# Kernel optimization log

Measured on AMD Instinct MI355X. Metric: run time of the kernel, lower is better.

## Reference

```python
import jax, jax.numpy as jnp
import numpy as np

D_MODEL = 1024
N_HEADS = 16
D_HEAD = D_MODEL // N_HEADS
EPS = 1e-6


def setup_inputs() -> dict:
    key = jax.random.key(0)
    ks = jax.random.split(key, 11)
    N, L, S = 4, 4096, 4096
    scale = 1.0 / np.sqrt(D_MODEL)
    inp = {
        "queries": jax.random.normal(ks[0], (N, L, D_MODEL), jnp.float32),
        "keys": jax.random.normal(ks[1], (N, S, D_MODEL), jnp.float32),
        "values": jax.random.normal(ks[2], (N, S, D_MODEL), jnp.float32),
        "Wq": jax.random.normal(ks[3], (D_MODEL, D_MODEL), jnp.float32) * scale,
        "bq": jnp.zeros((D_MODEL,), jnp.float32),
        "Wk": jax.random.normal(ks[4], (D_MODEL, D_MODEL), jnp.float32) * scale,
        "bk": jnp.zeros((D_MODEL,), jnp.float32),
        "Wv": jax.random.normal(ks[5], (D_MODEL, D_MODEL), jnp.float32) * scale,
        "bv": jnp.zeros((D_MODEL,), jnp.float32),
        "Wo": jax.random.normal(ks[6], (D_MODEL, D_MODEL), jnp.float32) * scale,
        "bo": jnp.zeros((D_MODEL,), jnp.float32),
    }
    return inp


def reference(queries, keys, values, Wq, bq, Wk, bk, Wv, bv, Wo, bo):
    N, L, _ = queries.shape
    S = keys.shape[1]
    H, Dh = N_HEADS, D_HEAD
    # projections (torch Linear: x @ W.T + b)
    q = (queries @ Wq.T + bq).reshape(N, L, H, Dh)
    k = (keys @ Wk.T + bk).reshape(N, S, H, Dh)
    v = (values @ Wv.T + bv).reshape(N, S, H, Dh)
    # elu+1 feature map
    Q = jax.nn.elu(q) + 1.0
    K = jax.nn.elu(k) + 1.0
    # KV summary: [N,H,Dv,Dh]
    KV = jnp.einsum('nshd,nshm->nhmd', K, v)
    # normalizer: [N,L,H]
    Z = 1.0 / (jnp.einsum('nlhd,nhd->nlh', Q, K.sum(axis=1)) + EPS)
    # output per head: [N,L,H,Dv]
    V = jnp.einsum('nlhd,nhmd,nlh->nlhm', Q, KV, Z)
    out = V.reshape(N, L, H * Dh) @ Wo.T + bo
    return out
```

## Files before the change

kernel.cpp:

```cpp
#include <hip/hip_runtime.h>
#include <hip/hip_bf16.h>

typedef __attribute__((ext_vector_type(8))) short short8;
typedef __attribute__((ext_vector_type(4))) short short4v;
typedef __attribute__((ext_vector_type(4))) float f32x4;

#define MFMA16(a, b, c) __builtin_amdgcn_mfma_f32_16x16x32_bf16(a, b, c, 0, 0, 0)

__device__ __forceinline__ unsigned short f2bf(float f) {
    unsigned int u = __float_as_uint(f);
    unsigned int r = u + 0x7fffu + ((u >> 16) & 1u);
    return (unsigned short)(r >> 16);
}
__device__ __forceinline__ float bf2f(unsigned short h) {
    return __uint_as_float(((unsigned int)h) << 16);
}

__device__ __forceinline__ void async16(const void* g, void* l) {
    __builtin_amdgcn_global_load_lds(
        (const __attribute__((address_space(1))) unsigned int*)g,
        (__attribute__((address_space(3))) unsigned int*)l, 16, 0, 0);
}

#define S_BARRIER() asm volatile("s_barrier" ::: "memory")
#define SCHED_FENCE() __builtin_amdgcn_sched_barrier(0)

__global__ __launch_bounds__(256) void cvt_kernel(const float* __restrict__ in,
                                                  unsigned short* __restrict__ out,
                                                  int n4) {
    int i = blockIdx.x * 256 + threadIdx.x;
    int stride = gridDim.x * 256;
    for (; i < n4; i += stride) {
        float4 v = reinterpret_cast<const float4*>(in)[i];
        short4v p;
        p[0] = (short)f2bf(v.x); p[1] = (short)f2bf(v.y);
        p[2] = (short)f2bf(v.z); p[3] = (short)f2bf(v.w);
        reinterpret_cast<short4v*>(out)[i] = p;
    }
}

template <int MODE>
__global__ __launch_bounds__(512, 2) void gemm8p(const unsigned short* __restrict__ A,
                                                 const unsigned short* __restrict__ B,
                                                 const float* __restrict__ bias,
                                                 void* __restrict__ out) {
    __shared__ __align__(16) char lds[131072];

    const int tid = threadIdx.x;
    const int lane = tid & 63, wid = tid >> 6;
    const int wr = wid >> 2, wc = wid & 3;
    const int lr = lane & 15, lg = lane >> 4;

    const int nwg = gridDim.x;
    const int bid = blockIdx.x;
    const int swz = (bid & 7) * (nwg >> 3) + (bid >> 3);
    const int bm = swz >> 2, bn = swz & 3;
    const long row0 = (long)bm * 256;
    const long col0 = (long)bn * 256;

    const unsigned short* srcA[2];
    const unsigned short* srcB[2];
    int dstOff[2];
#pragma unroll
    for (int g = 0; g < 2; ++g) {
        int s = g * 512 + tid;
        int pr = s >> 3;
        int dc = (s & 7) ^ (pr & 7);
        srcA[g] = A + (row0 + (pr & 63) + 128 * (pr >> 6)) * 1024 + dc * 8;
        srcB[g] = B + (col0 + pr) * 1024 + dc * 8;
        dstOff[g] = s * 16;
    }

#define STG_AQ(BB, Q, KT) do {                                                  \
        async16(srcA[0] + (Q) * 65536 + (KT) * 64,                              \
                lds + (BB) * 65536 + (Q) * 16384 + dstOff[0]);                  \
        async16(srcA[1] + (Q) * 65536 + (KT) * 64,                              \
                lds + (BB) * 65536 + (Q) * 16384 + dstOff[1]); } while (0)
#define STG_BH(BB, H, KT) do {                                                  \
        async16(srcB[0] + (H) * 131072 + (KT) * 64,                             \
                lds + (BB) * 65536 + 32768 + (H) * 16384 + dstOff[0]);          \
        async16(srcB[1] + (H) * 131072 + (KT) * 64,                             \
                lds + (BB) * 65536 + 32768 + (H) * 16384 + dstOff[1]); } while (0)

    const int ch0 = (((0 * 4 + lg) ^ (lr & 7)) << 4);
    const int ch1 = (((1 * 4 + lg) ^ (lr & 7)) << 4);
    const int aB0 = (64 * wr + lr) * 128 + ch0;
    const int aB1 = (64 * wr + lr) * 128 + ch1;
    const int bB0 = 32768 + (wc >> 1) * 16384 + ((wc & 1) * 64 + lr) * 128 + ch0;
    const int bB1 = 32768 + (wc >> 1) * 16384 + ((wc & 1) * 64 + lr) * 128 + ch1;

    f32x4 acc[8][4] = {};
    short8 b0[4], b1[4];

#define GATE4() do { asm volatile("s_waitcnt vmcnt(4)" ::: "memory"); SCHED_FENCE(); } while (0)
#define GATE0() do { asm volatile("s_waitcnt vmcnt(0)" ::: "memory"); SCHED_FENCE(); } while (0)
#define MFMA_BLOCK(MB, BV) do {                                                 \
        S_BARRIER();                                                            \
        asm volatile("s_waitcnt lgkmcnt(0)" ::: "memory");                      \
        SCHED_FENCE();                                                          \
        __builtin_amdgcn_s_setprio(1);                                          \
        _Pragma("unroll") for (int m = 0; m < 4; ++m)                           \
            _Pragma("unroll") for (int n = 0; n < 4; ++n)                       \
                acc[(MB) + m][n] = MFMA16(a[m], BV[n], acc[(MB) + m][n]);       \
        __builtin_amdgcn_s_setprio(0);                                          \
        SCHED_FENCE();                                                          \
        S_BARRIER(); } while (0)
#define LOAD_A(BUFB, ABASE, Q) do {                                             \
        _Pragma("unroll") for (int m = 0; m < 4; ++m)                           \
            a[m] = *(const short8*)(lds + (BUFB) + (Q) * 16384 + (ABASE) + m * 2048); } while (0)
#define LOAD_B(BUFB, BBASE, BV) do {                                            \
        _Pragma("unroll") for (int n = 0; n < 4; ++n)                           \
            BV[n] = *(const short8*)(lds + (BUFB) + (BBASE) + n * 2048); } while (0)

    STG_AQ(0, 0, 0); STG_BH(0, 0, 0); STG_BH(0, 1, 0); STG_AQ(0, 1, 0);
    STG_AQ(1, 0, 1); STG_BH(1, 0, 1);
    GATE4();
    S_BARRIER();

#pragma unroll 1
    for (int t = 0; t < 7; ++t) {
        const int ktA = 2 * t + 1, ktB = 2 * t + 2, ktC = 2 * t + 3;
        {
            short8 a[4];
            LOAD_B(0, bB0, b0); LOAD_A(0, aB0, 0);
            STG_BH(1, 1, ktA);
            MFMA_BLOCK(0, b0);
        }
        {
            short8 a[4];
            LOAD_B(0, bB1, b1); LOAD_A(0, aB1, 0);
            STG_AQ(1, 1, ktA);
            MFMA_BLOCK(0, b1);
        }
        {
            short8 a[4];
            LOAD_A(0, aB0, 1);
            STG_AQ(0, 0, ktB);
            MFMA_BLOCK(4, b0);
        }
        {
            short8 a[4];
            LOAD_A(0, aB1, 1);
            STG_BH(0, 0, ktB);
            GATE4();
            MFMA_BLOCK(4, b1);
        }
        {
            short8 a[4];
            LOAD_B(65536, bB0, b0); LOAD_A(65536, aB0, 0);
            STG_BH(0, 1, ktB);
            MFMA_BLOCK(0, b0);
        }
        {
            short8 a[4];
            LOAD_B(65536, bB1, b1); LOAD_A(65536, aB1, 0);
            STG_AQ(0, 1, ktB);
            MFMA_BLOCK(0, b1);
        }
        {
            short8 a[4];
            LOAD_A(65536, aB0, 1);
            STG_AQ(1, 0, ktC);
            MFMA_BLOCK(4, b0);
        }
        {
            short8 a[4];
            LOAD_A(65536, aB1, 1);
            STG_BH(1, 0, ktC);
            GATE4();
            MFMA_BLOCK(4, b1);
        }
    }
    {
        { short8 a[4]; LOAD_B(0, bB0, b0); LOAD_A(0, aB0, 0); STG_BH(1, 1, 15); MFMA_BLOCK(0, b0); }
        { short8 a[4]; LOAD_B(0, bB1, b1); LOAD_A(0, aB1, 0); STG_AQ(1, 1, 15); MFMA_BLOCK(0, b1); }
        { short8 a[4]; LOAD_A(0, aB0, 1); MFMA_BLOCK(4, b0); }
        { short8 a[4]; LOAD_A(0, aB1, 1); GATE0(); MFMA_BLOCK(4, b1); }
        { short8 a[4]; LOAD_B(65536, bB0, b0); LOAD_A(65536, aB0, 0); MFMA_BLOCK(0, b0); }
        { short8 a[4]; LOAD_B(65536, bB1, b1); LOAD_A(65536, aB1, 0); MFMA_BLOCK(0, b1); }
        { short8 a[4]; LOAD_A(65536, aB0, 1); MFMA_BLOCK(4, b0); }
        { short8 a[4]; LOAD_A(65536, aB1, 1); MFMA_BLOCK(4, b1); }
    }
#undef STG_AQ
#undef STG_BH
#undef GATE4
#undef GATE0
#undef MFMA_BLOCK
#undef LOAD_A
#undef LOAD_B

    const int r4 = lg * 4;
#pragma unroll
    for (int m = 0; m < 8; ++m) {
#pragma unroll
        for (int n = 0; n < 4; ++n) {
            long col = col0 + wc * 64 + n * 16 + lr;
            float bcol = bias[col];
            long R0 = row0 + wr * 128 + m * 16 + r4;
            if (MODE == 0) {
                unsigned short* O = (unsigned short*)out;
#pragma unroll
                for (int j = 0; j < 4; ++j) {
                    float v = acc[m][n][j] + bcol;
                    v = v > 0.f ? v + 1.f : __expf(v);
                    O[(R0 + j) * 1024 + col] = f2bf(v);
                }
            } else if (MODE == 1 || MODE == 2) {
                unsigned short* O = (unsigned short*)out;
                long nb = R0 >> 12;
                long s = R0 & 4095;
                short4v pack;
#pragma unroll
                for (int j = 0; j < 4; ++j) {
                    float v = acc[m][n][j] + bcol;
                    if (MODE == 1) v = v > 0.f ? v + 1.f : __expf(v);
                    pack[j] = (short)f2bf(v);
                }
                *(short4v*)(O + ((nb << 10) + col) * 4096 + s) = pack;
            } else {
                float* O = (float*)out;
#pragma unroll
                for (int j = 0; j < 4; ++j)
                    O[(R0 + j) * 1024 + col] = acc[m][n][j] + bcol;
            }
        }
    }
}

__global__ __launch_bounds__(256) void kv_kernel(const unsigned short* __restrict__ Kt,
                                                 const unsigned short* __restrict__ vT,
                                                 float* __restrict__ KV,
                                                 float* __restrict__ Ksum) {
    int b = blockIdx.x;
    int sc = b & 7, h = (b >> 3) & 15, n = b >> 7;
    const int tid = threadIdx.x, lane = tid & 63, wave = tid >> 6;
    long base = ((long)(n * 1024 + h * 64)) * 4096 + sc * 512;
    const unsigned short* Kp = Kt + base;
    const unsigned short* Vp = vT + base;
    const int lr = lane & 15, lk = (lane >> 4) * 8;

    f32x4 acc[4] = {};
    for (int s0 = 0; s0 < 512; s0 += 32) {
        short8 a = *(const short8*)(Vp + (long)(wave * 16 + lr) * 4096 + s0 + lk);
#pragma unroll
        for (int d4 = 0; d4 < 4; ++d4) {
            short8 bb = *(const short8*)(Kp + (long)(d4 * 16 + lr) * 4096 + s0 + lk);
            acc[d4] = MFMA16(a, bb, acc[d4]);
        }
    }
    float* KVb = KV + (long)(n * 16 + h) * 4096;
#pragma unroll
    for (int d4 = 0; d4 < 4; ++d4)
#pragma unroll
        for (int j = 0; j < 4; ++j) {
            int m = wave * 16 + (lane >> 4) * 4 + j;
            int d = d4 * 16 + lr;
            atomicAdd(KVb + m * 64 + d, acc[d4][j]);
        }
    int d = tid & 63, part = tid >> 6;
    const unsigned short* kp2 = Kt + ((long)(n * 1024 + h * 64 + d)) * 4096 + sc * 512 + part * 128;
    float s = 0.f;
    for (int i = 0; i < 128; i += 8) {
        short8 v = *(const short8*)(kp2 + i);
#pragma unroll
        for (int e = 0; e < 8; ++e) s += bf2f((unsigned short)v[e]);
    }
    atomicAdd(Ksum + n * 1024 + h * 64 + d, s);
}

__global__ __launch_bounds__(256) void attn_kernel(const unsigned short* __restrict__ Qm,
                                                   const float* __restrict__ KV,
                                                   const float* __restrict__ Ksum,
                                                   unsigned short* __restrict__ Vbuf) {
    __shared__ unsigned short Qs[128 * 64];
    __shared__ unsigned short KVs[64 * 64];
    __shared__ float zin[128];
    __shared__ float ks[64];
    int b = blockIdx.x;
    int lc = b & 31, h = (b >> 5) & 15, n = b >> 9;
    int tid = threadIdx.x, lane = tid & 63, wave = tid >> 6;
    long l0 = (long)n * 4096 + lc * 128;

    const unsigned short* Qg = Qm + (l0 + (tid >> 3)) * 1024 + h * 64 + (tid & 7) * 8;
    char* QsB = (char*)Qs + (wave << 10);
#pragma unroll
    for (int it = 0; it < 4; ++it)
        async16(Qg + (long)it * 32 * 1024, QsB + it * 4096);

    const float* kvp = KV + (long)(n * 16 + h) * 4096;
    for (int i = tid * 4; i < 4096; i += 1024) {
        float4 v = *reinterpret_cast<const float4*>(kvp + i);
        short4v p;
        p[0] = (short)f2bf(v.x); p[1] = (short)f2bf(v.y);
        p[2] = (short)f2bf(v.z); p[3] = (short)f2bf(v.w);
        *(short4v*)(KVs + i) = p;
    }
    if (tid < 64) ks[tid] = Ksum[n * 1024 + h * 64 + tid];
    __syncthreads();

    if (tid < 128) {
        float den = 0.f;
        const unsigned short* qrow = Qs + tid * 64;
#pragma unroll
        for (int d = 0; d < 64; ++d) den += bf2f(qrow[d]) * ks[d];
        zin[tid] = 1.0f / (den + 1e-6f);
    }
    __syncthreads();

    const int lr = lane & 15, lk = (lane >> 4) * 8;
    f32x4 acc[2][4] = {};
#pragma unroll
    for (int kk = 0; kk < 2; ++kk) {
        short8 a0 = *(const short8*)(Qs + (wave * 32 + lr) * 64 + kk * 32 + lk);
        short8 a1 = *(const short8*)(Qs + (wave * 32 + 16 + lr) * 64 + kk * 32 + lk);
#pragma unroll
        for (int nn = 0; nn < 4; ++nn) {
            short8 bb = *(const short8*)(KVs + (nn * 16 + lr) * 64 + kk * 32 + lk);
            acc[0][nn] = MFMA16(a0, bb, acc[0][nn]);
            acc[1][nn] = MFMA16(a1, bb, acc[1][nn]);
        }
    }
#pragma unroll
    for (int mi = 0; mi < 2; ++mi)
#pragma unroll
        for (int nn = 0; nn < 4; ++nn)
#pragma unroll
            for (int j = 0; j < 4; ++j) {
                int rl = wave * 32 + mi * 16 + (lane >> 4) * 4 + j;
                int mcol = nn * 16 + lr;
                float v = acc[mi][nn][j] * zin[rl];
                Vbuf[(l0 + rl) * 1024 + h * 64 + mcol] = f2bf(v);
            }
}

extern "C" void kernel_launch(void* const* d_in, const int* in_sizes, int n_in,
                              void* d_out, int out_size, void* d_ws, size_t ws_size,
                              hipStream_t stream) {
    const float* queries = (const float*)d_in[0];
    const float* keys    = (const float*)d_in[1];
    const float* values  = (const float*)d_in[2];
    const float* Wq = (const float*)d_in[3];
    const float* bq = (const float*)d_in[4];
    const float* Wk = (const float*)d_in[5];
    const float* bk = (const float*)d_in[6];
    const float* Wv = (const float*)d_in[7];
    const float* bv = (const float*)d_in[8];
    const float* Wo = (const float*)d_in[9];
    const float* bo = (const float*)d_in[10];
    float* out = (float*)d_out;

    char* ws = (char*)d_ws;
    const size_t SZ = (size_t)16384 * 1024 * 2;
    const size_t WSZ = (size_t)1024 * 1024 * 2;
    unsigned short* qb  = (unsigned short*)(ws);
    unsigned short* kb  = (unsigned short*)(ws + SZ);
    unsigned short* vb  = (unsigned short*)(ws + 2 * SZ);
    unsigned short* Wqb = (unsigned short*)(ws + 3 * SZ);
    unsigned short* Wkb = (unsigned short*)(ws + 3 * SZ + WSZ);
    unsigned short* Wvb = (unsigned short*)(ws + 3 * SZ + 2 * WSZ);
    unsigned short* Wob = (unsigned short*)(ws + 3 * SZ + 3 * WSZ);
    unsigned short* Qm  = (unsigned short*)(ws + 3 * SZ + 4 * WSZ);
    unsigned short* Kt  = (unsigned short*)(ws + 4 * SZ + 4 * WSZ);
    unsigned short* vT  = (unsigned short*)(ws + 5 * SZ + 4 * WSZ);
    float* KVf = (float*)(ws + 6 * SZ + 4 * WSZ);
    float* Ksf = (float*)(ws + 6 * SZ + 4 * WSZ + 1048576);
    unsigned short* Vbuf = qb;

    const int n4big = 16384 * 1024 / 4;
    const int n4w = 1024 * 1024 / 4;
    cvt_kernel<<<2048, 256, 0, stream>>>(queries, qb, n4big);
    cvt_kernel<<<2048, 256, 0, stream>>>(keys, kb, n4big);
    cvt_kernel<<<2048, 256, 0, stream>>>(values, vb, n4big);
    cvt_kernel<<<256, 256, 0, stream>>>(Wq, Wqb, n4w);
    cvt_kernel<<<256, 256, 0, stream>>>(Wk, Wkb, n4w);
    cvt_kernel<<<256, 256, 0, stream>>>(Wv, Wvb, n4w);
    cvt_kernel<<<256, 256, 0, stream>>>(Wo, Wob, n4w);

    gemm8p<0><<<256, 512, 0, stream>>>(qb, Wqb, bq, Qm);
    gemm8p<1><<<256, 512, 0, stream>>>(kb, Wkb, bk, Kt);
    gemm8p<2><<<256, 512, 0, stream>>>(vb, Wvb, bv, vT);

    hipMemsetAsync(KVf, 0, 1048576 + 16384, stream);
    kv_kernel<<<512, 256, 0, stream>>>(Kt, vT, KVf, Ksf);
    attn_kernel<<<2048, 256, 0, stream>>>(Qm, KVf, Ksf, Vbuf);

    gemm8p<3><<<256, 512, 0, stream>>>(Vbuf, Wob, bo, out);
}
```

Baseline: 273.0 us.

## Fuse fp32-to-bf16 activation conversion into projection GEMM A-tile loads

The Q/K/V projection GEMMs now read fp32 activations directly: each thread loads float4 pairs into registers, packs them to bf16 and writes them to LDS, which replaces the async global-to-LDS copies for the A operand. This drops three separate conversion kernels that each read 64MB of fp32 and wrote 32MB of bf16, along with the GEMM's later re-read of that bf16. The four weight conversions are also merged into one launch. The cost is register pressure from the prefetch buffers, extra VALU packing work inside the pipelined main loop, and double-width global reads for A.

```diff
diff --git a/kernel.cpp b/kernel.cpp
--- a/kernel.cpp
+++ b/kernel.cpp
@@ -15,6 +15,9 @@
 __device__ __forceinline__ float bf2f(unsigned short h) {
     return __uint_as_float(((unsigned int)h) << 16);
 }
+__device__ __forceinline__ unsigned int pk2(float lo, float hi) {
+    return (unsigned int)f2bf(lo) | ((unsigned int)f2bf(hi) << 16);
+}
 
 __device__ __forceinline__ void async16(const void* g, void* l) {
     __builtin_amdgcn_global_load_lds(
@@ -25,12 +28,20 @@
 #define S_BARRIER() asm volatile("s_barrier" ::: "memory")
 #define SCHED_FENCE() __builtin_amdgcn_sched_barrier(0)
 
-__global__ __launch_bounds__(256) void cvt_kernel(const float* __restrict__ in,
-                                                  unsigned short* __restrict__ out,
-                                                  int n4) {
-    int i = blockIdx.x * 256 + threadIdx.x;
-    int stride = gridDim.x * 256;
-    for (; i < n4; i += stride) {
+__global__ __launch_bounds__(256) void cvt4_kernel(const float* __restrict__ w0,
+                                                   const float* __restrict__ w1,
+                                                   const float* __restrict__ w2,
+                                                   const float* __restrict__ w3,
+                                                   unsigned short* __restrict__ o0,
+                                                   unsigned short* __restrict__ o1,
+                                                   unsigned short* __restrict__ o2,
+                                                   unsigned short* __restrict__ o3,
+                                                   int n4) {
+    int wsel = blockIdx.x >> 7;
+    int lb = blockIdx.x & 127;
+    const float* in = wsel == 0 ? w0 : wsel == 1 ? w1 : wsel == 2 ? w2 : w3;
+    unsigned short* out = wsel == 0 ? o0 : wsel == 1 ? o1 : wsel == 2 ? o2 : o3;
+    for (int i = lb * 256 + threadIdx.x; i < n4; i += 32768) {
         float4 v = reinterpret_cast<const float4*>(in)[i];
         short4v p;
         p[0] = (short)f2bf(v.x); p[1] = (short)f2bf(v.y);
@@ -39,8 +50,8 @@
     }
 }
 
-template <int MODE>
-__global__ __launch_bounds__(512, 2) void gemm8p(const unsigned short* __restrict__ A,
+template <int MODE, int AFP32>
+__global__ __launch_bounds__(512, 2) void gemm8p(const void* __restrict__ Araw,
                                                  const unsigned short* __restrict__ B,
                                                  const float* __restrict__ bias,
                                                  void* __restrict__ out) {
@@ -58,7 +69,8 @@
     const long row0 = (long)bm * 256;
     const long col0 = (long)bn * 256;
 
-    const unsigned short* srcA[2];
+    const int ESZ = AFP32 ? 4 : 2;
+    const char* srcAbase[2];
     const unsigned short* srcB[2];
     int dstOff[2];
 #pragma unroll
@@ -66,21 +78,35 @@
         int s = g * 512 + tid;
         int pr = s >> 3;
         int dc = (s & 7) ^ (pr & 7);
-        srcA[g] = A + (row0 + (pr & 63) + 128 * (pr >> 6)) * 1024 + dc * 8;
+        srcAbase[g] = (const char*)Araw +
+                      (long)((row0 + (pr & 63) + 128 * (pr >> 6)) * 1024 + dc * 8) * ESZ;
         srcB[g] = B + (col0 + pr) * 1024 + dc * 8;
         dstOff[g] = s * 16;
     }
 
 #define STG_AQ(BB, Q, KT) do {                                                  \
-        async16(srcA[0] + (Q) * 65536 + (KT) * 64,                              \
+        async16(srcAbase[0] + ((Q) * 65536 + (KT) * 64) * 2,                    \
                 lds + (BB) * 65536 + (Q) * 16384 + dstOff[0]);                  \
-        async16(srcA[1] + (Q) * 65536 + (KT) * 64,                              \
+        async16(srcAbase[1] + ((Q) * 65536 + (KT) * 64) * 2,                    \
                 lds + (BB) * 65536 + (Q) * 16384 + dstOff[1]); } while (0)
 #define STG_BH(BB, H, KT) do {                                                  \
         async16(srcB[0] + (H) * 131072 + (KT) * 64,                             \
                 lds + (BB) * 65536 + 32768 + (H) * 16384 + dstOff[0]);          \
         async16(srcB[1] + (H) * 131072 + (KT) * 64,                             \
                 lds + (BB) * 65536 + 32768 + (H) * 16384 + dstOff[1]); } while (0)
+#define A_ISSUE(ARR, Q, KT) do {                                                \
+        const char* s0_ = srcAbase[0] + ((Q) * 65536 + (KT) * 64) * 4;          \
+        const char* s1_ = srcAbase[1] + ((Q) * 65536 + (KT) * 64) * 4;          \
+        ARR[0] = *(const float4*)s0_;  ARR[1] = *(const float4*)(s0_ + 16);     \
+        ARR[2] = *(const float4*)s1_;  ARR[3] = *(const float4*)(s1_ + 16); } while (0)
+#define A_PACK(ARR, BB, Q) do {                                                 \
+        uint4 w0_, w1_;                                                         \
+        w0_.x = pk2(ARR[0].x, ARR[0].y); w0_.y = pk2(ARR[0].z, ARR[0].w);       \
+        w0_.z = pk2(ARR[1].x, ARR[1].y); w0_.w = pk2(ARR[1].z, ARR[1].w);       \
+        w1_.x = pk2(ARR[2].x, ARR[2].y); w1_.y = pk2(ARR[2].z, ARR[2].w);       \
+        w1_.z = pk2(ARR[3].x, ARR[3].y); w1_.w = pk2(ARR[3].z, ARR[3].w);       \
+        *(uint4*)(lds + (BB) * 65536 + (Q) * 16384 + dstOff[0]) = w0_;          \
+        *(uint4*)(lds + (BB) * 65536 + (Q) * 16384 + dstOff[1]) = w1_; } while (0)
 
     const int ch0 = (((0 * 4 + lg) ^ (lr & 7)) << 4);
     const int ch1 = (((1 * 4 + lg) ^ (lr & 7)) << 4);
@@ -91,8 +117,11 @@
 
     f32x4 acc[8][4] = {};
     short8 b0[4], b1[4];
-
-#define GATE4() do { asm volatile("s_waitcnt vmcnt(4)" ::: "memory"); SCHED_FENCE(); } while (0)
+    float4 apreA[4], apreB[4];
+
+#define GATEN() do { if (AFP32) asm volatile("s_waitcnt vmcnt(6)" ::: "memory");     \
+                     else       asm volatile("s_waitcnt vmcnt(4)" ::: "memory");     \
+                     SCHED_FENCE(); } while (0)
 #define GATE0() do { asm volatile("s_waitcnt vmcnt(0)" ::: "memory"); SCHED_FENCE(); } while (0)
 #define MFMA_BLOCK(MB, BV) do {                                                 \
         S_BARRIER();                                                            \
@@ -112,10 +141,24 @@
         _Pragma("unroll") for (int n = 0; n < 4; ++n)                           \
             BV[n] = *(const short8*)(lds + (BUFB) + (BBASE) + n * 2048); } while (0)
 
-    STG_AQ(0, 0, 0); STG_BH(0, 0, 0); STG_BH(0, 1, 0); STG_AQ(0, 1, 0);
-    STG_AQ(1, 0, 1); STG_BH(1, 0, 1);
-    GATE4();
-    S_BARRIER();
+    if (AFP32) {
+        STG_BH(0, 0, 0); STG_BH(0, 1, 0); STG_BH(1, 0, 1);
+        float4 t0[4], t1[4], t2[4];
+        A_ISSUE(t0, 0, 0); A_ISSUE(t1, 1, 0);
+        A_PACK(t0, 0, 0);
+        A_ISSUE(t2, 0, 1);
+        A_PACK(t1, 0, 1);
+        A_PACK(t2, 1, 0);
+        A_ISSUE(apreA, 1, 1);
+        asm volatile("s_waitcnt lgkmcnt(0)" ::: "memory");
+        SCHED_FENCE();
+        S_BARRIER();
+    } else {
+        STG_AQ(0, 0, 0); STG_BH(0, 0, 0); STG_BH(0, 1, 0); STG_AQ(0, 1, 0);
+        STG_AQ(1, 0, 1); STG_BH(1, 0, 1);
+        GATEN();
+        S_BARRIER();
+    }
 
 #pragma unroll 1
     for (int t = 0; t < 7; ++t) {
@@ -129,20 +172,22 @@
         {
             short8 a[4];
             LOAD_B(0, bB1, b1); LOAD_A(0, aB1, 0);
-            STG_AQ(1, 1, ktA);
+            if (AFP32) { A_ISSUE(apreB, 0, ktB); A_PACK(apreA, 1, 1); }
+            else       { STG_AQ(1, 1, ktA); }
             MFMA_BLOCK(0, b1);
         }
         {
             short8 a[4];
             LOAD_A(0, aB0, 1);
-            STG_AQ(0, 0, ktB);
+            if (AFP32) { A_ISSUE(apreA, 1, ktB); A_PACK(apreB, 0, 0); }
+            else       { STG_AQ(0, 0, ktB); }
             MFMA_BLOCK(4, b0);
         }
         {
             short8 a[4];
             LOAD_A(0, aB1, 1);
             STG_BH(0, 0, ktB);
-            GATE4();
+            GATEN();
             MFMA_BLOCK(4, b1);
         }
         {
@@ -154,26 +199,30 @@
         {
             short8 a[4];
             LOAD_B(65536, bB1, b1); LOAD_A(65536, aB1, 0);
-            STG_AQ(0, 1, ktB);
+            if (AFP32) { A_ISSUE(apreB, 0, ktC); A_PACK(apreA, 0, 1); }
+            else       { STG_AQ(0, 1, ktB); }
             MFMA_BLOCK(0, b1);
         }
         {
             short8 a[4];
             LOAD_A(65536, aB0, 1);
-            STG_AQ(1, 0, ktC);
+            if (AFP32) { A_ISSUE(apreA, 1, ktC); A_PACK(apreB, 1, 0); }
+            else       { STG_AQ(1, 0, ktC); }
             MFMA_BLOCK(4, b0);
         }
         {
             short8 a[4];
             LOAD_A(65536, aB1, 1);
             STG_BH(1, 0, ktC);
-            GATE4();
+            GATEN();
             MFMA_BLOCK(4, b1);
         }
     }
     {
         { short8 a[4]; LOAD_B(0, bB0, b0); LOAD_A(0, aB0, 0); STG_BH(1, 1, 15); MFMA_BLOCK(0, b0); }
-        { short8 a[4]; LOAD_B(0, bB1, b1); LOAD_A(0, aB1, 0); STG_AQ(1, 1, 15); MFMA_BLOCK(0, b1); }
+        { short8 a[4]; LOAD_B(0, bB1, b1); LOAD_A(0, aB1, 0);
+          if (AFP32) { A_PACK(apreA, 1, 1); } else { STG_AQ(1, 1, 15); }
+          MFMA_BLOCK(0, b1); }
         { short8 a[4]; LOAD_A(0, aB0, 1); MFMA_BLOCK(4, b0); }
         { short8 a[4]; LOAD_A(0, aB1, 1); GATE0(); MFMA_BLOCK(4, b1); }
         { short8 a[4]; LOAD_B(65536, bB0, b0); LOAD_A(65536, aB0, 0); MFMA_BLOCK(0, b0); }
@@ -183,7 +232,9 @@
     }
 #undef STG_AQ
 #undef STG_BH
-#undef GATE4
+#undef A_ISSUE
+#undef A_PACK
+#undef GATEN
 #undef GATE0
 #undef MFMA_BLOCK
 #undef LOAD_A
@@ -352,37 +403,27 @@
     char* ws = (char*)d_ws;
     const size_t SZ = (size_t)16384 * 1024 * 2;
     const size_t WSZ = (size_t)1024 * 1024 * 2;
-    unsigned short* qb  = (unsigned short*)(ws);
-    unsigned short* kb  = (unsigned short*)(ws + SZ);
-    unsigned short* vb  = (unsigned short*)(ws + 2 * SZ);
-    unsigned short* Wqb = (unsigned short*)(ws + 3 * SZ);
-    unsigned short* Wkb = (unsigned short*)(ws + 3 * SZ + WSZ);
-    unsigned short* Wvb = (unsigned short*)(ws + 3 * SZ + 2 * WSZ);
-    unsigned short* Wob = (unsigned short*)(ws + 3 * SZ + 3 * WSZ);
-    unsigned short* Qm  = (unsigned short*)(ws + 3 * SZ + 4 * WSZ);
-    unsigned short* Kt  = (unsigned short*)(ws + 4 * SZ + 4 * WSZ);
-    unsigned short* vT  = (unsigned short*)(ws + 5 * SZ + 4 * WSZ);
-    float* KVf = (float*)(ws + 6 * SZ + 4 * WSZ);
-    float* Ksf = (float*)(ws + 6 * SZ + 4 * WSZ + 1048576);
-    unsigned short* Vbuf = qb;
-
-    const int n4big = 16384 * 1024 / 4;
+    unsigned short* Wqb = (unsigned short*)(ws);
+    unsigned short* Wkb = (unsigned short*)(ws + WSZ);
+    unsigned short* Wvb = (unsigned short*)(ws + 2 * WSZ);
+    unsigned short* Wob = (unsigned short*)(ws + 3 * WSZ);
+    unsigned short* Qm   = (unsigned short*)(ws + 4 * WSZ);
+    unsigned short* Kt   = (unsigned short*)(ws + 4 * WSZ + SZ);
+    unsigned short* vT   = (unsigned short*)(ws + 4 * WSZ + 2 * SZ);
+    unsigned short* Vbuf = (unsigned short*)(ws + 4 * WSZ + 3 * SZ);
+    float* KVf = (float*)(ws + 4 * WSZ + 4 * SZ);
+    float* Ksf = (float*)(ws + 4 * WSZ + 4 * SZ + 1048576);
+
     const int n4w = 1024 * 1024 / 4;
-    cvt_kernel<<<2048, 256, 0, stream>>>(queries, qb, n4big);
-    cvt_kernel<<<2048, 256, 0, stream>>>(keys, kb, n4big);
-    cvt_kernel<<<2048, 256, 0, stream>>>(values, vb, n4big);
-    cvt_kernel<<<256, 256, 0, stream>>>(Wq, Wqb, n4w);
-    cvt_kernel<<<256, 256, 0, stream>>>(Wk, Wkb, n4w);
-    cvt_kernel<<<256, 256, 0, stream>>>(Wv, Wvb, n4w);
-    cvt_kernel<<<256, 256, 0, stream>>>(Wo, Wob, n4w);
-
-    gemm8p<0><<<256, 512, 0, stream>>>(qb, Wqb, bq, Qm);
-    gemm8p<1><<<256, 512, 0, stream>>>(kb, Wkb, bk, Kt);
-    gemm8p<2><<<256, 512, 0, stream>>>(vb, Wvb, bv, vT);
+    cvt4_kernel<<<512, 256, 0, stream>>>(Wq, Wk, Wv, Wo, Wqb, Wkb, Wvb, Wob, n4w);
+
+    gemm8p<0, 1><<<256, 512, 0, stream>>>(queries, Wqb, bq, Qm);
+    gemm8p<1, 1><<<256, 512, 0, stream>>>(keys, Wkb, bk, Kt);
+    gemm8p<2, 1><<<256, 512, 0, stream>>>(values, Wvb, bv, vT);
 
     hipMemsetAsync(KVf, 0, 1048576 + 16384, stream);
     kv_kernel<<<512, 256, 0, stream>>>(Kt, vT, KVf, Ksf);
     attn_kernel<<<2048, 256, 0, stream>>>(Qm, KVf, Ksf, Vbuf);
 
-    gemm8p<3><<<256, 512, 0, stream>>>(Vbuf, Wob, bo, out);
-}
+    gemm8p<3, 0><<<256, 512, 0, stream>>>(Vbuf, Wob, bo, out);
+}
```

Result: slower. 289.9 us (+6.2%).

## Merge conversion launches and batch Q/K/V projection GEMMs into single kernels

Applied to the files above, without the earlier changes.

Replaces seven separate fp32-to-bf16 conversion launches with one kernel that dispatches by block index, and merges the three projection GEMMs into one 768-block launch that picks its operands per segment. This is meant to remove launch gaps and tail underutilization between the small kernels. The GEMM body becomes a device function with a runtime mode, which may add branching in the epilogue. Launch bounds change from 2 to 1 blocks per SM. The attention kernel also spreads the normalizer dot product across all 256 threads with a shuffle reduction instead of 128 threads.

```diff
diff --git a/kernel.cpp b/kernel.cpp
--- a/kernel.cpp
+++ b/kernel.cpp
@@ -25,35 +25,56 @@
 #define S_BARRIER() asm volatile("s_barrier" ::: "memory")
 #define SCHED_FENCE() __builtin_amdgcn_sched_barrier(0)
 
-__global__ __launch_bounds__(256) void cvt_kernel(const float* __restrict__ in,
-                                                  unsigned short* __restrict__ out,
-                                                  int n4) {
-    int i = blockIdx.x * 256 + threadIdx.x;
-    int stride = gridDim.x * 256;
-    for (; i < n4; i += stride) {
-        float4 v = reinterpret_cast<const float4*>(in)[i];
+__global__ __launch_bounds__(256) void cvt_all(const float* __restrict__ q,
+                                               const float* __restrict__ k,
+                                               const float* __restrict__ v,
+                                               const float* __restrict__ Wq,
+                                               const float* __restrict__ Wk,
+                                               const float* __restrict__ Wv,
+                                               const float* __restrict__ Wo,
+                                               unsigned short* __restrict__ qb,
+                                               unsigned short* __restrict__ kb,
+                                               unsigned short* __restrict__ vb,
+                                               unsigned short* __restrict__ Wqb,
+                                               unsigned short* __restrict__ Wkb,
+                                               unsigned short* __restrict__ Wvb,
+                                               unsigned short* __restrict__ Wob) {
+    int b = blockIdx.x;
+    const float* in;
+    unsigned short* out;
+    int lb, nb, n4;
+    if (b < 6144) {
+        int s = b >> 11;
+        lb = b & 2047; nb = 2048; n4 = 4194304;
+        in = s == 0 ? q : s == 1 ? k : v;
+        out = s == 0 ? qb : s == 1 ? kb : vb;
+    } else {
+        int s = b - 6144;
+        int w = s >> 7;
+        lb = s & 127; nb = 128; n4 = 262144;
+        in = w == 0 ? Wq : w == 1 ? Wk : w == 2 ? Wv : Wo;
+        out = w == 0 ? Wqb : w == 1 ? Wkb : w == 2 ? Wvb : Wob;
+    }
+    for (int i = lb * 256 + threadIdx.x; i < n4; i += nb * 256) {
+        float4 vv = reinterpret_cast<const float4*>(in)[i];
         short4v p;
-        p[0] = (short)f2bf(v.x); p[1] = (short)f2bf(v.y);
-        p[2] = (short)f2bf(v.z); p[3] = (short)f2bf(v.w);
+        p[0] = (short)f2bf(vv.x); p[1] = (short)f2bf(vv.y);
+        p[2] = (short)f2bf(vv.z); p[3] = (short)f2bf(vv.w);
         reinterpret_cast<short4v*>(out)[i] = p;
     }
 }
 
-template <int MODE>
-__global__ __launch_bounds__(512, 2) void gemm8p(const unsigned short* __restrict__ A,
-                                                 const unsigned short* __restrict__ B,
-                                                 const float* __restrict__ bias,
-                                                 void* __restrict__ out) {
-    __shared__ __align__(16) char lds[131072];
-
+__device__ __forceinline__ void gemm_body(const unsigned short* __restrict__ A,
+                                          const unsigned short* __restrict__ B,
+                                          const float* __restrict__ bias,
+                                          void* __restrict__ out,
+                                          int mode, char* lds, int bid) {
     const int tid = threadIdx.x;
     const int lane = tid & 63, wid = tid >> 6;
     const int wr = wid >> 2, wc = wid & 3;
     const int lr = lane & 15, lg = lane >> 4;
 
-    const int nwg = gridDim.x;
-    const int bid = blockIdx.x;
-    const int swz = (bid & 7) * (nwg >> 3) + (bid >> 3);
+    const int swz = (bid & 7) * 32 + (bid >> 3);
     const int bm = swz >> 2, bn = swz & 3;
     const long row0 = (long)bm * 256;
     const long col0 = (long)bn * 256;
@@ -120,56 +141,14 @@
 #pragma unroll 1
     for (int t = 0; t < 7; ++t) {
         const int ktA = 2 * t + 1, ktB = 2 * t + 2, ktC = 2 * t + 3;
-        {
-            short8 a[4];
-            LOAD_B(0, bB0, b0); LOAD_A(0, aB0, 0);
-            STG_BH(1, 1, ktA);
-            MFMA_BLOCK(0, b0);
-        }
-        {
-            short8 a[4];
-            LOAD_B(0, bB1, b1); LOAD_A(0, aB1, 0);
-            STG_AQ(1, 1, ktA);
-            MFMA_BLOCK(0, b1);
-        }
-        {
-            short8 a[4];
-            LOAD_A(0, aB0, 1);
-            STG_AQ(0, 0, ktB);
-            MFMA_BLOCK(4, b0);
-        }
-        {
-            short8 a[4];
-            LOAD_A(0, aB1, 1);
-            STG_BH(0, 0, ktB);
-            GATE4();
-            MFMA_BLOCK(4, b1);
-        }
-        {
-            short8 a[4];
-            LOAD_B(65536, bB0, b0); LOAD_A(65536, aB0, 0);
-            STG_BH(0, 1, ktB);
-            MFMA_BLOCK(0, b0);
-        }
-        {
-            short8 a[4];
-            LOAD_B(65536, bB1, b1); LOAD_A(65536, aB1, 0);
-            STG_AQ(0, 1, ktB);
-            MFMA_BLOCK(0, b1);
-        }
-        {
-            short8 a[4];
-            LOAD_A(65536, aB0, 1);
-            STG_AQ(1, 0, ktC);
-            MFMA_BLOCK(4, b0);
-        }
-        {
-            short8 a[4];
-            LOAD_A(65536, aB1, 1);
-            STG_BH(1, 0, ktC);
-            GATE4();
-            MFMA_BLOCK(4, b1);
-        }
+        { short8 a[4]; LOAD_B(0, bB0, b0); LOAD_A(0, aB0, 0); STG_BH(1, 1, ktA); MFMA_BLOCK(0, b0); }
+        { short8 a[4]; LOAD_B(0, bB1, b1); LOAD_A(0, aB1, 0); STG_AQ(1, 1, ktA); MFMA_BLOCK(0, b1); }
+        { short8 a[4]; LOAD_A(0, aB0, 1); STG_AQ(0, 0, ktB); MFMA_BLOCK(4, b0); }
+        { short8 a[4]; LOAD_A(0, aB1, 1); STG_BH(0, 0, ktB); GATE4(); MFMA_BLOCK(4, b1); }
+        { short8 a[4]; LOAD_B(65536, bB0, b0); LOAD_A(65536, aB0, 0); STG_BH(0, 1, ktB); MFMA_BLOCK(0, b0); }
+        { short8 a[4]; LOAD_B(65536, bB1, b1); LOAD_A(65536, aB1, 0); STG_AQ(0, 1, ktB); MFMA_BLOCK(0, b1); }
+        { short8 a[4]; LOAD_A(65536, aB0, 1); STG_AQ(1, 0, ktC); MFMA_BLOCK(4, b0); }
+        { short8 a[4]; LOAD_A(65536, aB1, 1); STG_BH(1, 0, ktC); GATE4(); MFMA_BLOCK(4, b1); }
     }
     {
         { short8 a[4]; LOAD_B(0, bB0, b0); LOAD_A(0, aB0, 0); STG_BH(1, 1, 15); MFMA_BLOCK(0, b0); }
@@ -197,7 +176,7 @@
             long col = col0 + wc * 64 + n * 16 + lr;
             float bcol = bias[col];
             long R0 = row0 + wr * 128 + m * 16 + r4;
-            if (MODE == 0) {
+            if (mode == 0) {
                 unsigned short* O = (unsigned short*)out;
 #pragma unroll
                 for (int j = 0; j < 4; ++j) {
@@ -205,7 +184,7 @@
                     v = v > 0.f ? v + 1.f : __expf(v);
                     O[(R0 + j) * 1024 + col] = f2bf(v);
                 }
-            } else if (MODE == 1 || MODE == 2) {
+            } else if (mode == 1 || mode == 2) {
                 unsigned short* O = (unsigned short*)out;
                 long nb = R0 >> 12;
                 long s = R0 & 4095;
@@ -213,7 +192,7 @@
 #pragma unroll
                 for (int j = 0; j < 4; ++j) {
                     float v = acc[m][n][j] + bcol;
-                    if (MODE == 1) v = v > 0.f ? v + 1.f : __expf(v);
+                    if (mode == 1) v = v > 0.f ? v + 1.f : __expf(v);
                     pack[j] = (short)f2bf(v);
                 }
                 *(short4v*)(O + ((nb << 10) + col) * 4096 + s) = pack;
@@ -225,6 +204,36 @@
             }
         }
     }
+}
+
+__global__ __launch_bounds__(512, 1) void proj_gemm(const unsigned short* __restrict__ qb,
+                                                    const unsigned short* __restrict__ kb,
+                                                    const unsigned short* __restrict__ vb,
+                                                    const unsigned short* __restrict__ Wqb,
+                                                    const unsigned short* __restrict__ Wkb,
+                                                    const unsigned short* __restrict__ Wvb,
+                                                    const float* __restrict__ bq,
+                                                    const float* __restrict__ bk,
+                                                    const float* __restrict__ bv,
+                                                    unsigned short* __restrict__ Qm,
+                                                    unsigned short* __restrict__ Kt,
+                                                    unsigned short* __restrict__ vT) {
+    __shared__ __align__(16) char lds[131072];
+    int seg = blockIdx.x >> 8;
+    int bid = blockIdx.x & 255;
+    const unsigned short* A = seg == 0 ? qb : seg == 1 ? kb : vb;
+    const unsigned short* B = seg == 0 ? Wqb : seg == 1 ? Wkb : Wvb;
+    const float* bias = seg == 0 ? bq : seg == 1 ? bk : bv;
+    void* out = seg == 0 ? (void*)Qm : seg == 1 ? (void*)Kt : (void*)vT;
+    gemm_body(A, B, bias, out, seg, lds, bid);
+}
+
+__global__ __launch_bounds__(512, 1) void out_gemm(const unsigned short* __restrict__ Vbuf,
+                                                   const unsigned short* __restrict__ Wob,
+                                                   const float* __restrict__ bo,
+                                                   float* __restrict__ out) {
+    __shared__ __align__(16) char lds[131072];
+    gemm_body(Vbuf, Wob, bo, out, 3, lds, blockIdx.x);
 }
 
 __global__ __launch_bounds__(256) void kv_kernel(const unsigned short* __restrict__ Kt,
@@ -298,12 +307,14 @@
     if (tid < 64) ks[tid] = Ksum[n * 1024 + h * 64 + tid];
     __syncthreads();
 
-    if (tid < 128) {
+    {
+        int row = tid >> 1, half = tid & 1;
         float den = 0.f;
-        const unsigned short* qrow = Qs + tid * 64;
-#pragma unroll
-        for (int d = 0; d < 64; ++d) den += bf2f(qrow[d]) * ks[d];
-        zin[tid] = 1.0f / (den + 1e-6f);
+        const unsigned short* qrow = Qs + row * 64 + half * 32;
+#pragma unroll
+        for (int d = 0; d < 32; ++d) den += bf2f(qrow[d]) * ks[half * 32 + d];
+        den += __shfl_xor(den, 1, 64);
+        if (half == 0) zin[row] = 1.0f / (den + 1e-6f);
     }
     __syncthreads();
 
@@ -366,23 +377,14 @@
     float* Ksf = (float*)(ws + 6 * SZ + 4 * WSZ + 1048576);
     unsigned short* Vbuf = qb;
 
-    const int n4big = 16384 * 1024 / 4;
-    const int n4w = 1024 * 1024 / 4;
-    cvt_kernel<<<2048, 256, 0, stream>>>(queries, qb, n4big);
-    cvt_kernel<<<2048, 256, 0, stream>>>(keys, kb, n4big);
-    cvt_kernel<<<2048, 256, 0, stream>>>(values, vb, n4big);
-    cvt_kernel<<<256, 256, 0, stream>>>(Wq, Wqb, n4w);
-    cvt_kernel<<<256, 256, 0, stream>>>(Wk, Wkb, n4w);
-    cvt_kernel<<<256, 256, 0, stream>>>(Wv, Wvb, n4w);
-    cvt_kernel<<<256, 256, 0, stream>>>(Wo, Wob, n4w);
-
-    gemm8p<0><<<256, 512, 0, stream>>>(qb, Wqb, bq, Qm);
-    gemm8p<1><<<256, 512, 0, stream>>>(kb, Wkb, bk, Kt);
-    gemm8p<2><<<256, 512, 0, stream>>>(vb, Wvb, bv, vT);
+    cvt_all<<<6656, 256, 0, stream>>>(queries, keys, values, Wq, Wk, Wv, Wo,
+                                      qb, kb, vb, Wqb, Wkb, Wvb, Wob);
+
+    proj_gemm<<<768, 512, 0, stream>>>(qb, kb, vb, Wqb, Wkb, Wvb, bq, bk, bv, Qm, Kt, vT);
 
     hipMemsetAsync(KVf, 0, 1048576 + 16384, stream);
     kv_kernel<<<512, 256, 0, stream>>>(Kt, vT, KVf, Ksf);
     attn_kernel<<<2048, 256, 0, stream>>>(Qm, KVf, Ksf, Vbuf);
 
-    gemm8p<3><<<256, 512, 0, stream>>>(Vbuf, Wob, bo, out);
-}
+    out_gemm<<<256, 512, 0, stream>>>(Vbuf, Wob, bo, out);
+}
```

Result: faster. 257.0 us (-5.9%).
